# Kernel tuning notes

Measured on AMD Instinct MI355X. Metric: run time of the kernel, lower is better.

The kernel has to match this reference:

```python
import jax, jax.numpy as jnp
import numpy as np

DMODEL = 1024
NHEADS = 16
FFN = 4 * DMODEL
HEAD_DIM = DMODEL // NHEADS
SCALE = HEAD_DIM ** -0.5


def layer_norm(x, gamma, beta, eps=1e-5):
    mu = jnp.mean(x, axis=-1, keepdims=True)
    var = jnp.var(x, axis=-1, keepdims=True)
    return (x - mu) * jax.lax.rsqrt(var + eps) * gamma + beta


def setup_inputs() -> dict:
    key = jax.random.key(0)
    ks = jax.random.split(key, 8)
    std = 0.02
    B, S = 2, 2048
    return {
        "src": jax.random.normal(ks[0], (B, S, DMODEL), jnp.float32),
        "pre_gamma": jnp.ones((DMODEL,), jnp.float32),
        "pre_beta": jnp.zeros((DMODEL,), jnp.float32),
        "qkv_w": jax.random.truncated_normal(ks[1], -2.0, 2.0, (3 * DMODEL, DMODEL), jnp.float32) * std,
        "qkv_b": jnp.zeros((3 * DMODEL,), jnp.float32),
        "addnorm_gamma": jnp.ones((DMODEL,), jnp.float32),
        "addnorm_beta": jnp.zeros((DMODEL,), jnp.float32),
        "fc1_w": jax.random.truncated_normal(ks[2], -2.0, 2.0, (FFN, DMODEL), jnp.float32) * std,
        "fc1_b": jnp.zeros((FFN,), jnp.float32),
        "fc2_w": jax.random.truncated_normal(ks[3], -2.0, 2.0, (DMODEL, FFN), jnp.float32) * std,
        "fc2_b": jnp.zeros((DMODEL,), jnp.float32),
    }


def reference(src, pre_gamma, pre_beta, qkv_w, qkv_b, addnorm_gamma, addnorm_beta,
              fc1_w, fc1_b, fc2_w, fc2_b):
    B, S, D = src.shape
    # PreNorm
    x = layer_norm(src, pre_gamma, pre_beta)
    # MHSA (no output projection, matching source)
    qkv = x @ qkv_w.T + qkv_b  # [B,S,3D]
    q, k, v = jnp.split(qkv, 3, axis=-1)
    def heads(t):
        return t.reshape(B, S, NHEADS, HEAD_DIM).transpose(0, 2, 1, 3)  # [B,H,S,hd]
    q, k, v = heads(q), heads(k), heads(v)
    attn = jnp.einsum("bhqd,bhkd->bhqk", q, k) * SCALE
    attn = jax.nn.softmax(attn, axis=-1)
    attn_out = jnp.einsum("bhqk,bhkd->bhqd", attn, v)
    attn_out = attn_out.transpose(0, 2, 1, 3).reshape(B, S, D)
    # shared AddNorm #1
    x = layer_norm(attn_out + x, addnorm_gamma, addnorm_beta)
    # FFN
    h = jax.nn.gelu(x @ fc1_w.T + fc1_b, approximate=False)
    ffn_out = h @ fc2_w.T + fc2_b
    # shared AddNorm #2 (same params as #1)
    return layer_norm(ffn_out + x, addnorm_gamma, addnorm_beta)
```

## Files before the change

### kernel.cpp

```cpp
#include <hip/hip_runtime.h>
#include <hip/hip_bf16.h>
#include <math.h>

#define DMODEL 1024
#define NH 16
#define HD 64
#define SEQ 2048
#define BATCH 2
#define MROWS (BATCH * SEQ)
#define FFN_DIM 4096

using bf16x8 = __attribute__((ext_vector_type(8))) __bf16;
using f32x4  = __attribute__((ext_vector_type(4))) float;

typedef const __attribute__((address_space(1))) unsigned char* gas_t;
typedef __attribute__((address_space(3))) unsigned char* las_t;

__device__ inline unsigned short f2bf(float f) {
    unsigned int u = __builtin_bit_cast(unsigned int, f);
    u += 0x7fffu + ((u >> 16) & 1u);
    return (unsigned short)(u >> 16);
}
__device__ inline unsigned short f2bf_up(float f) {
    unsigned int u = __builtin_bit_cast(unsigned int, f);
    return (unsigned short)((u + 0x8000u) >> 16);
}
__device__ inline float bf2f(unsigned short u) {
    unsigned int v = ((unsigned int)u) << 16;
    return __builtin_bit_cast(float, v);
}
__device__ inline float gelu_f(float x) {
    float x2 = x * x;
    float w = x * fmaf(0.07135481627f, x2, 1.59576912161f);
    return x / (1.0f + __expf(-w));
}

__global__ __launch_bounds__(256) void ln_pre_cvt(
        const float* __restrict__ a,
        const float* __restrict__ gamma, const float* __restrict__ beta,
        float* __restrict__ out_f, unsigned short* __restrict__ out_b,
        const float* __restrict__ wa, unsigned short* __restrict__ oa, int na4,
        const float* __restrict__ wb, unsigned short* __restrict__ ob, int nb4,
        const float* __restrict__ wc, unsigned char* __restrict__ oc, int nc4) {
    int blk = blockIdx.x;
    int t = threadIdx.x;
    if (blk >= MROWS) {
        int i = (blk - MROWS) * 256 + t;
        if (i < na4) {
            float4 v = ((const float4*)wa)[i];
            ushort4 o;
            o.x = f2bf(v.x); o.y = f2bf(v.y); o.z = f2bf(v.z); o.w = f2bf(v.w);
            ((ushort4*)oa)[i] = o;
        } else if (i < na4 + nb4) {
            int j = i - na4;
            float4 v = ((const float4*)wb)[j];
            ushort4 o;
            o.x = f2bf(v.x); o.y = f2bf(v.y); o.z = f2bf(v.z); o.w = f2bf(v.w);
            ((ushort4*)ob)[j] = o;
        } else if (i < na4 + nb4 + nc4) {
            int j = i - na4 - nb4;
            float4 v = ((const float4*)wc)[j];
            int pk = __builtin_amdgcn_cvt_pk_fp8_f32(v.x, v.y, 0, false);
            pk     = __builtin_amdgcn_cvt_pk_fp8_f32(v.z, v.w, pk, true);
            ((unsigned int*)oc)[j] = (unsigned int)pk;
        }
        return;
    }
    int row = blk;
    float4 v = ((const float4*)(a + (size_t)row * DMODEL))[t];
    float s  = v.x + v.y + v.z + v.w;
    float s2 = v.x * v.x + v.y * v.y + v.z * v.z + v.w * v.w;
    #pragma unroll
    for (int off = 32; off > 0; off >>= 1) {
        s  += __shfl_xor(s,  off, 64);
        s2 += __shfl_xor(s2, off, 64);
    }
    __shared__ float red[8];
    int wave = t >> 6, lane = t & 63;
    if (lane == 0) { red[wave] = s; red[4 + wave] = s2; }
    __syncthreads();
    float tot  = red[0] + red[1] + red[2] + red[3];
    float tot2 = red[4] + red[5] + red[6] + red[7];
    float mu   = tot * (1.0f / DMODEL);
    float var  = tot2 * (1.0f / DMODEL) - mu * mu;
    float rstd = rsqrtf(var + 1e-5f);
    float4 g  = ((const float4*)gamma)[t];
    float4 be = ((const float4*)beta)[t];
    float4 o;
    o.x = (v.x - mu) * rstd * g.x + be.x;
    o.y = (v.y - mu) * rstd * g.y + be.y;
    o.z = (v.z - mu) * rstd * g.z + be.z;
    o.w = (v.w - mu) * rstd * g.w + be.w;
    ((float4*)(out_f + (size_t)row * DMODEL))[t] = o;
    ushort4 ob4;
    ob4.x = f2bf(o.x); ob4.y = f2bf(o.y); ob4.z = f2bf(o.z); ob4.w = f2bf(o.w);
    ((ushort4*)(out_b + (size_t)row * DMODEL))[t] = ob4;
}

__global__ __launch_bounds__(256) void ln_attn(
        const float* __restrict__ o0, const float* __restrict__ o1,
        const float* __restrict__ l0, const float* __restrict__ l1,
        const float* __restrict__ xres,
        const float* __restrict__ gamma, const float* __restrict__ beta,
        float* __restrict__ out_f, unsigned short* __restrict__ out_b) {
    int row = blockIdx.x;
    int t = threadIdx.x;
    int b_ = row >> 11, s = row & 2047;
    int h = t >> 4;
    int bh = b_ * NH + h;
    size_t obase = ((size_t)bh * SEQ + s) * HD + (4 * t & 63);
    float4 va = ((const float4*)(o0 + obase))[0];
    float4 vb = ((const float4*)(o1 + obase))[0];
    float inv_l = 1.0f / (l0[(size_t)bh * SEQ + s] + l1[(size_t)bh * SEQ + s]);
    float4 rr = ((const float4*)(xres + (size_t)row * DMODEL))[t];
    float4 v;
    v.x = (va.x + vb.x) * inv_l + rr.x;
    v.y = (va.y + vb.y) * inv_l + rr.y;
    v.z = (va.z + vb.z) * inv_l + rr.z;
    v.w = (va.w + vb.w) * inv_l + rr.w;

    float s1 = v.x + v.y + v.z + v.w;
    float s2 = v.x * v.x + v.y * v.y + v.z * v.z + v.w * v.w;
    #pragma unroll
    for (int off = 32; off > 0; off >>= 1) {
        s1 += __shfl_xor(s1, off, 64);
        s2 += __shfl_xor(s2, off, 64);
    }
    __shared__ float red[8];
    int wave = t >> 6, lane = t & 63;
    if (lane == 0) { red[wave] = s1; red[4 + wave] = s2; }
    __syncthreads();
    float tot  = red[0] + red[1] + red[2] + red[3];
    float tot2 = red[4] + red[5] + red[6] + red[7];
    float mu   = tot * (1.0f / DMODEL);
    float var  = tot2 * (1.0f / DMODEL) - mu * mu;
    float rstd = rsqrtf(var + 1e-5f);
    float4 g  = ((const float4*)gamma)[t];
    float4 be = ((const float4*)beta)[t];
    float4 o;
    o.x = (v.x - mu) * rstd * g.x + be.x;
    o.y = (v.y - mu) * rstd * g.y + be.y;
    o.z = (v.z - mu) * rstd * g.z + be.z;
    o.w = (v.w - mu) * rstd * g.w + be.w;
    ((float4*)(out_f + (size_t)row * DMODEL))[t] = o;
    ushort4 ob;
    ob.x = f2bf(o.x); ob.y = f2bf(o.y); ob.z = f2bf(o.z); ob.w = f2bf(o.w);
    ((ushort4*)(out_b + (size_t)row * DMODEL))[t] = ob;
}

__global__ __launch_bounds__(256) void ln_fc2(
        const unsigned short* __restrict__ p0, const unsigned short* __restrict__ p1,
        const unsigned short* __restrict__ p2, const unsigned short* __restrict__ p3,
        const float* __restrict__ bias, const float* __restrict__ resid,
        const float* __restrict__ gamma, const float* __restrict__ beta,
        float* __restrict__ out_f) {
    int row = blockIdx.x;
    int t = threadIdx.x;
    size_t base = (size_t)row * DMODEL;
    ushort4 u0 = ((const ushort4*)(p0 + base))[t];
    ushort4 u1 = ((const ushort4*)(p1 + base))[t];
    ushort4 u2 = ((const ushort4*)(p2 + base))[t];
    ushort4 u3 = ((const ushort4*)(p3 + base))[t];
    float4 bb = ((const float4*)bias)[t];
    float4 rr = ((const float4*)(resid + base))[t];
    float4 v;
    v.x = bf2f(u0.x) + bf2f(u1.x) + bf2f(u2.x) + bf2f(u3.x) + bb.x + rr.x;
    v.y = bf2f(u0.y) + bf2f(u1.y) + bf2f(u2.y) + bf2f(u3.y) + bb.y + rr.y;
    v.z = bf2f(u0.z) + bf2f(u1.z) + bf2f(u2.z) + bf2f(u3.z) + bb.z + rr.z;
    v.w = bf2f(u0.w) + bf2f(u1.w) + bf2f(u2.w) + bf2f(u3.w) + bb.w + rr.w;

    float s  = v.x + v.y + v.z + v.w;
    float s2 = v.x * v.x + v.y * v.y + v.z * v.z + v.w * v.w;
    #pragma unroll
    for (int off = 32; off > 0; off >>= 1) {
        s  += __shfl_xor(s,  off, 64);
        s2 += __shfl_xor(s2, off, 64);
    }
    __shared__ float red[8];
    int wave = t >> 6, lane = t & 63;
    if (lane == 0) { red[wave] = s; red[4 + wave] = s2; }
    __syncthreads();
    float tot  = red[0] + red[1] + red[2] + red[3];
    float tot2 = red[4] + red[5] + red[6] + red[7];
    float mu   = tot * (1.0f / DMODEL);
    float var  = tot2 * (1.0f / DMODEL) - mu * mu;
    float rstd = rsqrtf(var + 1e-5f);
    float4 g  = ((const float4*)gamma)[t];
    float4 be = ((const float4*)beta)[t];
    float4 o;
    o.x = (v.x - mu) * rstd * g.x + be.x;
    o.y = (v.y - mu) * rstd * g.y + be.y;
    o.z = (v.z - mu) * rstd * g.z + be.z;
    o.w = (v.w - mu) * rstd * g.w + be.w;
    ((float4*)(out_f + base))[t] = o;
}

template <int MODE>
__global__ __launch_bounds__(256) void gemm_lds(
        const unsigned short* __restrict__ A,
        const unsigned short* __restrict__ Bw,
        const float* __restrict__ bias,
        void* __restrict__ out, int M, int N, int K) {
    __shared__ unsigned short As[2][128 * 64];
    __shared__ unsigned short Bs[2][128 * 64];

    const int tid  = threadIdx.x;
    const int wave = tid >> 6;
    const int lane = tid & 63;
    const int quad = lane >> 4;
    const int cc   = lane & 15;
    const int bn = blockIdx.x * 128;
    const int bm = blockIdx.y * 128;

    const unsigned short* Ab = A  + (size_t)bm * K;
    const unsigned short* Bb = Bw + (size_t)bn * K;

    const int srow0 = tid >> 3;
    const int sslot = tid & 7;
    const int rsw   = (cc >> 1) & 7;
    const int wm = (wave >> 1) * 64;
    const int wn = (wave & 1) * 64;

    f32x4 acc[4][4] = {};

    auto stage = [&](int buf, int k0) {
        #pragma unroll
        for (int i = 0; i < 4; ++i) {
            int row = i * 32 + srow0;
            int g   = sslot ^ ((row >> 1) & 7);
            const unsigned short* ga = Ab + (size_t)row * K + k0 + g * 8;
            const unsigned short* gb = Bb + (size_t)row * K + k0 + g * 8;
            unsigned short* la = &As[buf][i * 2048 + wave * 512];
            unsigned short* lb = &Bs[buf][i * 2048 + wave * 512];
            __builtin_amdgcn_global_load_lds((gas_t)(const void*)ga, (las_t)(void*)la, 16, 0, 0);
            __builtin_amdgcn_global_load_lds((gas_t)(const void*)gb, (las_t)(void*)lb, 16, 0, 0);
        }
    };

    const int nkt = K >> 6;
    stage(0, 0);
    __syncthreads();

    int cur = 0;
    for (int kt = 0; kt < nkt; ++kt) {
        if (kt + 1 < nkt) stage(cur ^ 1, (kt + 1) << 6);

        bf16x8 af[4][2], bf[4][2];
        #pragma unroll
        for (int mt = 0; mt < 4; ++mt)
            #pragma unroll
            for (int s = 0; s < 2; ++s) {
                int slot = (s * 4 + quad) ^ rsw;
                af[mt][s] = *(const bf16x8*)&As[cur][(wm + mt * 16 + cc) * 64 + slot * 8];
            }
        #pragma unroll
        for (int nt = 0; nt < 4; ++nt)
            #pragma unroll
            for (int s = 0; s < 2; ++s) {
                int slot = (s * 4 + quad) ^ rsw;
                bf[nt][s] = *(const bf16x8*)&Bs[cur][(wn + nt * 16 + cc) * 64 + slot * 8];
            }

        #pragma unroll
        for (int mt = 0; mt < 4; ++mt)
            #pragma unroll
            for (int nt = 0; nt < 4; ++nt) {
                acc[mt][nt] = __builtin_amdgcn_mfma_f32_16x16x32_bf16(
                    af[mt][0], bf[nt][0], acc[mt][nt], 0, 0, 0);
                acc[mt][nt] = __builtin_amdgcn_mfma_f32_16x16x32_bf16(
                    af[mt][1], bf[nt][1], acc[mt][nt], 0, 0, 0);
            }

        if (kt + 1 < nkt) __syncthreads();
        cur ^= 1;
    }

    #pragma unroll
    for (int mt = 0; mt < 4; ++mt)
        #pragma unroll
        for (int nt = 0; nt < 4; ++nt) {
            if constexpr (MODE == 1) {
                int m0 = bm + wm + mt * 16 + quad * 4;
                int n  = bn + wn + nt * 16 + cc;
                float bn_ = bias[n];
                float v0 = gelu_f(acc[mt][nt][0] + bn_);
                float v1 = gelu_f(acc[mt][nt][1] + bn_);
                float v2 = gelu_f(acc[mt][nt][2] + bn_);
                float v3 = gelu_f(acc[mt][nt][3] + bn_);
                int pk = __builtin_amdgcn_cvt_pk_fp8_f32(v0, v1, 0, false);
                pk     = __builtin_amdgcn_cvt_pk_fp8_f32(v2, v3, pk, true);
                unsigned char* o = (unsigned char*)out + (size_t)m0 * N + n;
                o[0]             = (unsigned char)pk;
                o[(size_t)N]     = (unsigned char)(pk >> 8);
                o[(size_t)2 * N] = (unsigned char)(pk >> 16);
                o[(size_t)3 * N] = (unsigned char)(pk >> 24);
            } else {
                #pragma unroll
                for (int r = 0; r < 4; ++r) {
                    int m = bm + wm + mt * 16 + quad * 4 + r;
                    int n = bn + wn + nt * 16 + cc;
                    float v = acc[mt][nt][r] + bias[n];
                    int b_ = m >> 11, srow = m & 2047;
                    int which = n >> 10, rem = n & 1023;
                    int h = rem >> 6, d = rem & 63;
                    if (which == 0) v *= 0.125f;
                    size_t idx = ((((size_t)which * BATCH + b_) * NH + h) * SEQ + srow) * HD + d;
                    ((unsigned short*)out)[idx] = f2bf(v);
                }
            }
        }
}

__global__ __launch_bounds__(256) void gemm_fp8(
        const unsigned char* __restrict__ A,
        const unsigned char* __restrict__ Bw,
        unsigned short* __restrict__ p0, unsigned short* __restrict__ p1,
        unsigned short* __restrict__ p2, unsigned short* __restrict__ p3,
        int M, int N, int K, int KC) {
    __shared__ unsigned char As[2][128 * 64];
    __shared__ unsigned char Bs[2][128 * 64];

    const int tid  = threadIdx.x;
    const int wave = tid >> 6;
    const int lane = tid & 63;
    const int quad = lane >> 4;
    const int cc   = lane & 15;
    const int bn = blockIdx.x * 128;
    const int bm = blockIdx.y * 128;

    const unsigned char* Ab = A  + (size_t)bm * K;
    const unsigned char* Bb = Bw + (size_t)bn * K;

    const int srow0 = tid >> 2;
    const int schunk = tid & 3;
    const int rsw = (cc >> 1) & 3;
    const int wm = (wave >> 1) * 64;
    const int wn = (wave & 1) * 64;

    const int kbeg = blockIdx.z * KC;

    f32x4 acc[4][4] = {};

    auto stage = [&](int buf, int k0) {
        #pragma unroll
        for (int i = 0; i < 2; ++i) {
            int row = i * 64 + srow0;
            int g   = schunk ^ ((row >> 1) & 3);
            const unsigned char* ga = Ab + (size_t)row * K + k0 + g * 16;
            const unsigned char* gb = Bb + (size_t)row * K + k0 + g * 16;
            unsigned char* la = &As[buf][i * 4096 + wave * 1024];
            unsigned char* lb = &Bs[buf][i * 4096 + wave * 1024];
            __builtin_amdgcn_global_load_lds((gas_t)(const void*)ga, (las_t)(void*)la, 16, 0, 0);
            __builtin_amdgcn_global_load_lds((gas_t)(const void*)gb, (las_t)(void*)lb, 16, 0, 0);
        }
    };

    const int nkt = KC >> 6;
    stage(0, kbeg);
    __syncthreads();

    int cur = 0;
    for (int kt = 0; kt < nkt; ++kt) {
        if (kt + 1 < nkt) stage(cur ^ 1, kbeg + ((kt + 1) << 6));

        long af[4][2], bf[4][2];
        #pragma unroll
        for (int mt = 0; mt < 4; ++mt)
            #pragma unroll
            for (int s = 0; s < 2; ++s) {
                int slot = ((quad >> 1) + 2 * s) ^ rsw;
                af[mt][s] = *(const long*)&As[cur][(wm + mt * 16 + cc) * 64 + slot * 16 + (quad & 1) * 8];
            }
        #pragma unroll
        for (int nt = 0; nt < 4; ++nt)
            #pragma unroll
            for (int s = 0; s < 2; ++s) {
                int slot = ((quad >> 1) + 2 * s) ^ rsw;
                bf[nt][s] = *(const long*)&Bs[cur][(wn + nt * 16 + cc) * 64 + slot * 16 + (quad & 1) * 8];
            }

        #pragma unroll
        for (int mt = 0; mt < 4; ++mt)
            #pragma unroll
            for (int nt = 0; nt < 4; ++nt) {
                acc[mt][nt] = __builtin_amdgcn_mfma_f32_16x16x32_fp8_fp8(
                    af[mt][0], bf[nt][0], acc[mt][nt], 0, 0, 0);
                acc[mt][nt] = __builtin_amdgcn_mfma_f32_16x16x32_fp8_fp8(
                    af[mt][1], bf[nt][1], acc[mt][nt], 0, 0, 0);
            }

        if (kt + 1 < nkt) __syncthreads();
        cur ^= 1;
    }

    unsigned short* outp = (blockIdx.z == 0) ? p0
                         : (blockIdx.z == 1) ? p1
                         : (blockIdx.z == 2) ? p2 : p3;
    #pragma unroll
    for (int mt = 0; mt < 4; ++mt)
        #pragma unroll
        for (int nt = 0; nt < 4; ++nt)
            #pragma unroll
            for (int r = 0; r < 4; ++r) {
                int m = bm + wm + mt * 16 + quad * 4 + r;
                int n = bn + wn + nt * 16 + cc;
                outp[(size_t)m * N + n] = f2bf(acc[mt][nt][r]);
            }
}

__global__ __launch_bounds__(256) void transpose_v(
        const unsigned short* __restrict__ vsrc, unsigned short* __restrict__ vt) {
    __shared__ unsigned short Ls[64 * 72];
    const int t = threadIdx.x;
    const int s0 = blockIdx.x * 64;
    const int bh = blockIdx.y;
    const unsigned short* in = vsrc + (size_t)bh * SEQ * HD;
    unsigned short* outp = vt + (size_t)bh * SEQ * HD;

    const int row = t >> 2;
    const int c8  = (t & 3) * 8;
    #pragma unroll
    for (int p = 0; p < 2; ++p)
        *(uint4*)&Ls[row * 72 + c8 + p * 32] =
            *(const uint4*)&in[(size_t)(s0 + row) * HD + c8 + p * 32];
    __syncthreads();

    const int hd = t >> 2;
    #pragma unroll
    for (int p = 0; p < 2; ++p) {
        unsigned short tmp[8];
        #pragma unroll
        for (int j = 0; j < 8; ++j)
            tmp[j] = Ls[(c8 + p * 32 + j) * 72 + hd];
        *(uint4*)&outp[(size_t)hd * SEQ + s0 + c8 + p * 32] = *(uint4*)tmp;
    }
}

#define KPAD 72
__global__ __launch_bounds__(256, 4) void attn_mfma(
        const unsigned short* __restrict__ qkv,
        const unsigned short* __restrict__ vt,
        float* __restrict__ op0, float* __restrict__ op1,
        float* __restrict__ lpart) {
    const int tid  = threadIdx.x;
    const int wave = tid >> 6;
    const int lane = tid & 63;
    const int quad = lane >> 4;
    const int cc   = lane & 15;
    const int qblk = blockIdx.x;
    const int bh   = blockIdx.y;
    const int half = blockIdx.z;

    const size_t headsz = (size_t)SEQ * HD;
    const unsigned short* qb  = qkv + (size_t)bh * headsz;
    const unsigned short* kb  = qkv + ((size_t)BATCH * NH + bh) * headsz;
    const unsigned short* vtb = vt + (size_t)bh * headsz;
    float* opart = half ? op1 : op0;
    float* lp    = lpart + (size_t)half * BATCH * NH * SEQ;

    __shared__ unsigned short Ks[64 * KPAD];
    __shared__ unsigned short Vt[64 * KPAD];
    __shared__ unsigned short Ps[4 * 32 * KPAD];

    bf16x8 qa[2][2];
    #pragma unroll
    for (int mt = 0; mt < 2; ++mt) {
        const unsigned short* qp =
            qb + (size_t)(qblk * 128 + wave * 32 + mt * 16 + cc) * HD + quad * 8;
        qa[mt][0] = *(const bf16x8*)qp;
        qa[mt][1] = *(const bf16x8*)(qp + 32);
    }

    f32x4 o_acc[2][4] = {};
    float l_i[2][4] = {};

    const int srow = wave * 16 + (lane >> 2);
    const int sc8  = (lane & 3) * 8;
    const int psw  = (cc >> 2) & 3;

    for (int kt = half * 16; kt < half * 16 + 16; ++kt) {
        __syncthreads();
        #pragma unroll
        for (int p = 0; p < 2; ++p) {
            int col = sc8 + p * 32;
            *(uint4*)&Ks[srow * KPAD + col] =
                *(const uint4*)&kb[(size_t)(kt * 64 + srow) * HD + col];
            *(uint4*)&Vt[srow * KPAD + col] =
                *(const uint4*)&vtb[(size_t)srow * SEQ + kt * 64 + col];
        }
        __syncthreads();

        f32x4 s_acc[2][4];
        #pragma unroll
        for (int nt = 0; nt < 4; ++nt) {
            const unsigned short* kp = &Ks[(nt * 16 + cc) * KPAD + quad * 8];
            bf16x8 kf0 = *(const bf16x8*)kp;
            bf16x8 kf1 = *(const bf16x8*)(kp + 32);
            #pragma unroll
            for (int mt = 0; mt < 2; ++mt) {
                f32x4 z = {};
                z = __builtin_amdgcn_mfma_f32_16x16x32_bf16(qa[mt][0], kf0, z, 0, 0, 0);
                s_acc[mt][nt] = __builtin_amdgcn_mfma_f32_16x16x32_bf16(qa[mt][1], kf1, z, 0, 0, 0);
            }
        }

        unsigned short* pw = &Ps[wave * 32 * KPAD];
        #pragma unroll
        for (int mt = 0; mt < 2; ++mt)
            #pragma unroll
            for (int nt = 0; nt < 4; ++nt) {
                int pc = ((nt ^ quad) & 3) * 16 + cc;
                #pragma unroll
                for (int r = 0; r < 4; ++r) {
                    float e = __expf(s_acc[mt][nt][r]);
                    l_i[mt][r] += e;
                    pw[(mt * 16 + quad * 4 + r) * KPAD + pc] = f2bf_up(e);
                }
            }

        bf16x8 pf[2][2];
        #pragma unroll
        for (int mt = 0; mt < 2; ++mt) {
            const unsigned short* pa = &pw[(mt * 16 + cc) * KPAD];
            pf[mt][0] = *(const bf16x8*)&pa[((((quad >> 1))     ^ psw) & 3) * 16 + (quad & 1) * 8];
            pf[mt][1] = *(const bf16x8*)&pa[(((2 + (quad >> 1)) ^ psw) & 3) * 16 + (quad & 1) * 8];
        }

        #pragma unroll
        for (int nt = 0; nt < 4; ++nt) {
            const unsigned short* vp = &Vt[(nt * 16 + cc) * KPAD + quad * 8];
            bf16x8 vf0 = *(const bf16x8*)vp;
            bf16x8 vf1 = *(const bf16x8*)(vp + 32);
            #pragma unroll
            for (int mt = 0; mt < 2; ++mt) {
                o_acc[mt][nt] = __builtin_amdgcn_mfma_f32_16x16x32_bf16(
                    pf[mt][0], vf0, o_acc[mt][nt], 0, 0, 0);
                o_acc[mt][nt] = __builtin_amdgcn_mfma_f32_16x16x32_bf16(
                    pf[mt][1], vf1, o_acc[mt][nt], 0, 0, 0);
            }
        }
    }

    #pragma unroll
    for (int mt = 0; mt < 2; ++mt) {
        float lr[4];
        #pragma unroll
        for (int r = 0; r < 4; ++r) {
            float l = l_i[mt][r];
            #pragma unroll
            for (int off = 1; off < 16; off <<= 1)
                l += __shfl_xor(l, off, 64);
            lr[r] = l;
        }
        int rowbase = qblk * 128 + wave * 32 + mt * 16;
        if (cc == 0) {
            float4 lv = {lr[0], lr[1], lr[2], lr[3]};
            *(float4*)&lp[(size_t)bh * SEQ + rowbase + quad * 4] = lv;
        }
        #pragma unroll
        for (int nt = 0; nt < 4; ++nt)
            #pragma unroll
            for (int r = 0; r < 4; ++r) {
                int row = rowbase + quad * 4 + r;
                opart[((size_t)bh * SEQ + row) * HD + nt * 16 + cc] = o_acc[mt][nt][r];
            }
    }
}

extern "C" void kernel_launch(void* const* d_in, const int* in_sizes, int n_in,
                              void* d_out, int out_size, void* d_ws, size_t ws_size,
                              hipStream_t stream) {
    const float* src       = (const float*)d_in[0];
    const float* pre_gamma = (const float*)d_in[1];
    const float* pre_beta  = (const float*)d_in[2];
    const float* qkv_w     = (const float*)d_in[3];
    const float* qkv_b     = (const float*)d_in[4];
    const float* an_gamma  = (const float*)d_in[5];
    const float* an_beta   = (const float*)d_in[6];
    const float* fc1_w     = (const float*)d_in[7];
    const float* fc1_b     = (const float*)d_in[8];
    const float* fc2_w     = (const float*)d_in[9];
    const float* fc2_b     = (const float*)d_in[10];
    float* out = (float*)d_out;

    char* ws = (char*)d_ws;
    size_t off = 0;
    auto alloc = [&](size_t bytes) {
        char* p = ws + off;
        off += (bytes + 255) & ~(size_t)255;
        return p;
    };
    float*          x_f   = (float*)alloc((size_t)MROWS * DMODEL * 4);
    unsigned short* x_b   = (unsigned short*)alloc((size_t)MROWS * DMODEL * 2);
    float*          y_f   = (float*)alloc((size_t)MROWS * DMODEL * 4);
    unsigned short* y_b   = (unsigned short*)alloc((size_t)MROWS * DMODEL * 2);
    float*          atf   = (float*)alloc((size_t)MROWS * DMODEL * 4);
    float*          fff   = (float*)alloc((size_t)MROWS * DMODEL * 4);
    unsigned short* qkvb  = (unsigned short*)alloc((size_t)3 * MROWS * DMODEL * 2);
    unsigned char*  h8    = (unsigned char*)alloc((size_t)MROWS * FFN_DIM * 2);
    unsigned short* wqkv  = (unsigned short*)alloc((size_t)3 * DMODEL * DMODEL * 2);
    unsigned short* wfc1  = (unsigned short*)alloc((size_t)FFN_DIM * DMODEL * 2);
    unsigned char*  wfc28 = (unsigned char*)alloc((size_t)DMODEL * FFN_DIM);

    unsigned short* vt_b = (unsigned short*)fff;
    float* opart0 = atf;
    float* opart1 = (float*)h8;
    float* lpart  = (float*)x_b;
    unsigned short* fc2p0 = (unsigned short*)fff;
    unsigned short* fc2p1 = (unsigned short*)x_f;
    unsigned short* fc2p2 = (unsigned short*)atf;
    unsigned short* fc2p3 = (unsigned short*)qkvb;

    int n_qkv4 = 3 * DMODEL * DMODEL / 4;
    int n_fc4  = FFN_DIM * DMODEL / 4;
    int cvt_blocks = (n_qkv4 + 2 * n_fc4 + 255) / 256;

    ln_pre_cvt<<<dim3(MROWS + cvt_blocks), dim3(256), 0, stream>>>(
        src, pre_gamma, pre_beta, x_f, x_b,
        qkv_w, wqkv, n_qkv4, fc1_w, wfc1, n_fc4, fc2_w, wfc28, n_fc4);

    gemm_lds<3><<<dim3(3 * DMODEL / 128, MROWS / 128), dim3(256), 0, stream>>>(
        x_b, wqkv, qkv_b, qkvb, MROWS, 3 * DMODEL, DMODEL);
    transpose_v<<<dim3(SEQ / 64, BATCH * NH), dim3(256), 0, stream>>>(
        qkvb + (size_t)2 * BATCH * NH * SEQ * HD, vt_b);
    attn_mfma<<<dim3(SEQ / 128, BATCH * NH, 2), dim3(256), 0, stream>>>(
        qkvb, vt_b, opart0, opart1, lpart);
    ln_attn<<<dim3(MROWS), dim3(256), 0, stream>>>(
        opart0, opart1, lpart, lpart + (size_t)BATCH * NH * SEQ,
        x_f, an_gamma, an_beta, y_f, y_b);
    gemm_lds<1><<<dim3(FFN_DIM / 128, MROWS / 128), dim3(256), 0, stream>>>(
        y_b, wfc1, fc1_b, h8, MROWS, FFN_DIM, DMODEL);
    gemm_fp8<<<dim3(DMODEL / 128, MROWS / 128, 4), dim3(256), 0, stream>>>(
        h8, wfc28, fc2p0, fc2p1, fc2p2, fc2p3, MROWS, DMODEL, FFN_DIM, 1024);
    ln_fc2<<<dim3(MROWS), dim3(256), 0, stream>>>(
        fc2p0, fc2p1, fc2p2, fc2p3, fc2_b, y_f, an_gamma, an_beta, out);
}
```

Baseline: 323.6 us.

## Load K/V fragments directly from global with XCD-aware block swizzle in attention

The attention kernel no longer stages K and V tiles through shared memory behind two barriers per tile. Each wave instead reads its MFMA operand fragments straight from global memory. The 3D grid is flattened and remapped so that all 16 query blocks of one head/half land on the same XCD, letting them share K/V through that XCD's L2. This removes the LDS copy and barrier cost, but every wave now fetches K/V redundantly and depends on cache hits and global latency with no explicit prefetch.

Measured after the change: 386.9 us. 1.2x slower.

```diff
diff --git a/kernel.cpp b/kernel.cpp
--- a/kernel.cpp
+++ b/kernel.cpp
@@ -447,9 +447,14 @@
     const int lane = tid & 63;
     const int quad = lane >> 4;
     const int cc   = lane & 15;
-    const int qblk = blockIdx.x;
-    const int bh   = blockIdx.y;
-    const int half = blockIdx.z;
+
+    const int L    = blockIdx.x;
+    const int xcd  = L & 7;
+    const int idx  = L >> 3;
+    const int grp  = xcd + 8 * (idx >> 4);
+    const int qblk = idx & 15;
+    const int bh   = grp & 31;
+    const int half = grp >> 5;
 
     const size_t headsz = (size_t)SEQ * HD;
     const unsigned short* qb  = qkv + (size_t)bh * headsz;
@@ -458,8 +463,6 @@
     float* opart = half ? op1 : op0;
     float* lp    = lpart + (size_t)half * BATCH * NH * SEQ;
 
-    __shared__ unsigned short Ks[64 * KPAD];
-    __shared__ unsigned short Vt[64 * KPAD];
     __shared__ unsigned short Ps[4 * 32 * KPAD];
 
     bf16x8 qa[2][2];
@@ -474,26 +477,14 @@
     f32x4 o_acc[2][4] = {};
     float l_i[2][4] = {};
 
-    const int srow = wave * 16 + (lane >> 2);
-    const int sc8  = (lane & 3) * 8;
-    const int psw  = (cc >> 2) & 3;
+    const int psw = (cc >> 2) & 3;
 
     for (int kt = half * 16; kt < half * 16 + 16; ++kt) {
-        __syncthreads();
-        #pragma unroll
-        for (int p = 0; p < 2; ++p) {
-            int col = sc8 + p * 32;
-            *(uint4*)&Ks[srow * KPAD + col] =
-                *(const uint4*)&kb[(size_t)(kt * 64 + srow) * HD + col];
-            *(uint4*)&Vt[srow * KPAD + col] =
-                *(const uint4*)&vtb[(size_t)srow * SEQ + kt * 64 + col];
-        }
-        __syncthreads();
-
         f32x4 s_acc[2][4];
         #pragma unroll
         for (int nt = 0; nt < 4; ++nt) {
-            const unsigned short* kp = &Ks[(nt * 16 + cc) * KPAD + quad * 8];
+            const unsigned short* kp =
+                kb + (size_t)(kt * 64 + nt * 16 + cc) * HD + quad * 8;
             bf16x8 kf0 = *(const bf16x8*)kp;
             bf16x8 kf1 = *(const bf16x8*)(kp + 32);
             #pragma unroll
@@ -528,7 +519,8 @@
 
         #pragma unroll
         for (int nt = 0; nt < 4; ++nt) {
-            const unsigned short* vp = &Vt[(nt * 16 + cc) * KPAD + quad * 8];
+            const unsigned short* vp =
+                vtb + (size_t)(nt * 16 + cc) * SEQ + kt * 64 + quad * 8;
             bf16x8 vf0 = *(const bf16x8*)vp;
             bf16x8 vf1 = *(const bf16x8*)(vp + 32);
             #pragma unroll
@@ -623,7 +615,7 @@
         x_b, wqkv, qkv_b, qkvb, MROWS, 3 * DMODEL, DMODEL);
     transpose_v<<<dim3(SEQ / 64, BATCH * NH), dim3(256), 0, stream>>>(
         qkvb + (size_t)2 * BATCH * NH * SEQ * HD, vt_b);
-    attn_mfma<<<dim3(SEQ / 128, BATCH * NH, 2), dim3(256), 0, stream>>>(
+    attn_mfma<<<dim3(SEQ / 128 * BATCH * NH * 2), dim3(256), 0, stream>>>(
         qkvb, vt_b, opart0, opart1, lpart);
     ln_attn<<<dim3(MROWS), dim3(256), 0, stream>>>(
         opart0, opart1, lpart, lpart + (size_t)BATCH * NH * SEQ,
```
